# Optimization experiments

Measured on AMD Instinct MI355X. Metric: run time of the kernel, lower is better.

The kernel has to match this reference:

```python
import jax, jax.numpy as jnp
import numpy as np

B, C, D, H, W = 4, 128, 16, 16, 16
C8 = C // 8
TEXT = 256
N = D * H * W


def setup_inputs() -> dict:
    key = jax.random.key(0)
    ks = jax.random.split(key, 13)
    s = lambda fan: 1.0 / np.sqrt(fan)
    return {
        "x": jax.random.normal(ks[0], (B, C, D, H, W), jnp.float32),
        "text_emb": jax.random.normal(ks[1], (B, TEXT), jnp.float32),
        "Wq": jax.random.normal(ks[2], (C8, C), jnp.float32) * s(C),
        "bq": jax.random.normal(ks[3], (C8,), jnp.float32) * 0.01,
        "Wk": jax.random.normal(ks[4], (C8, C), jnp.float32) * s(C),
        "bk": jax.random.normal(ks[5], (C8,), jnp.float32) * 0.01,
        "Wv": jax.random.normal(ks[6], (C, C), jnp.float32) * s(C),
        "bv": jax.random.normal(ks[7], (C,), jnp.float32) * 0.01,
        "Wtk": jax.random.normal(ks[8], (C8, TEXT), jnp.float32) * s(TEXT),
        "btk": jax.random.normal(ks[9], (C8,), jnp.float32) * 0.01,
        "Wtv": jax.random.normal(ks[10], (C, TEXT), jnp.float32) * s(TEXT),
        "btv": jax.random.normal(ks[11], (C,), jnp.float32) * 0.01,
        # gamma is zero-init in the original; use a nonzero value so the
        # attention path contributes to the output (and to gradients).
        "gamma": jax.random.normal(ks[12], (1,), jnp.float32) * 0.1 + 0.5,
    }


def reference(x, text_emb, Wq, bq, Wk, bk, Wv, bv, Wtk, btk, Wtv, btv, gamma):
    b, c, d, h, w = x.shape
    n = d * h * w
    xf = x.reshape(b, c, n)                       # [B, C, N]
    # 1x1x1 convs == channel matmuls
    q = jnp.einsum('oc,bcn->bno', Wq, xf) + bq    # [B, N, C8]
    k = jnp.einsum('oc,bcn->bon', Wk, xf) + bk[None, :, None]  # [B, C8, N]
    v = jnp.einsum('oc,bcn->bon', Wv, xf) + bv[None, :, None]  # [B, C, N]
    # text-conditioned additive key/value (broadcast over all voxels)
    tk = (text_emb @ Wtk.T + btk)[:, :, None]     # [B, C8, 1]
    tv = (text_emb @ Wtv.T + btv)[:, :, None]     # [B, C, 1]
    k = k + tk
    v = v + tv
    # unscaled attention: softmax over keys
    scores = jnp.einsum('bno,bom->bnm', q, k)     # [B, N, N]
    attn = jax.nn.softmax(scores, axis=-1)
    # out[b,c,n] = sum_m v[b,c,m] * attn[b,n,m]
    out = jnp.einsum('bcm,bnm->bcn', v, attn).reshape(b, c, d, h, w)
    return gamma * out + x
```

## Files before the change

kernel.cpp:

```cpp
#include <hip/hip_runtime.h>
#include <math.h>

#define BB 4
#define CC 128
#define C8 16
#define TEXTN 256
#define NN 4096
#define WQB 64
#define NT 32

typedef __attribute__((ext_vector_type(8))) __bf16 bf16x8;
typedef __attribute__((ext_vector_type(16))) float f32x16;

#define LOG2E 1.44269504088896340736f

static __device__ __forceinline__ ushort f2bf(float f) {
  unsigned u = __builtin_bit_cast(unsigned, f);
  u += 0x7FFFu + ((u >> 16) & 1u);
  return (ushort)(u >> 16);
}

static __device__ __forceinline__ float exp2a(float x) {
#if __has_builtin(__builtin_amdgcn_exp2f)
  return __builtin_amdgcn_exp2f(x);
#else
  return exp2f(x);
#endif
}

static __device__ __forceinline__ unsigned cvt_pk_bf16(float lo, float hi) {
  unsigned r;
  asm("v_cvt_pk_bf16_f32 %0, %1, %2" : "=v"(r) : "v"(lo), "v"(hi));
  return r;
}
static __device__ __forceinline__ void pl32swap(unsigned &a, unsigned &b) {
  asm("v_permlane32_swap_b32 %0, %1" : "+v"(a), "+v"(b));
}

#define SB() __builtin_amdgcn_sched_barrier(0)

__global__ __launch_bounds__(256) void k_text(
    const float* __restrict__ text, const float* __restrict__ Wtk,
    const float* __restrict__ btk, const float* __restrict__ Wtv,
    const float* __restrict__ btv, float* __restrict__ tkv) {
  __shared__ float ts[TEXTN];
  int b = blockIdx.x;
  for (int i = threadIdx.x; i < TEXTN; i += 256) ts[i] = text[b * TEXTN + i];
  __syncthreads();
  int o = threadIdx.x;
  if (o < 144) {
    const float* w;
    float acc;
    if (o < 16) { w = Wtk + o * TEXTN; acc = btk[o]; }
    else        { w = Wtv + (o - 16) * TEXTN; acc = btv[o - 16]; }
    #pragma unroll 8
    for (int t = 0; t < TEXTN; t++) acc += w[t] * ts[t];
    tkv[b * 144 + o] = acc;
  }
}

__global__ __launch_bounds__(320) void k_qkv(
    const float* __restrict__ x,
    const float* __restrict__ Wq, const float* __restrict__ bq,
    const float* __restrict__ Wk, const float* __restrict__ bk,
    const float* __restrict__ Wv, const float* __restrict__ bv,
    const float* __restrict__ tkv,
    ushort* __restrict__ qt, ushort* __restrict__ kt, ushort* __restrict__ vtB) {
  __shared__ __align__(16) ushort xs[64 * 128];
  int b = blockIdx.x >> 6;
  int n0 = (blockIdx.x & 63) * 64;
  int t = threadIdx.x;
  int w = t >> 6, lane = t & 63, l31 = lane & 31, hi = lane >> 5;

  for (int i = t; i < 1024; i += 320) {
    int n = i & 63, ch = i >> 6;
    union { ushort u[8]; uint4 v; } pk;
    #pragma unroll
    for (int j = 0; j < 8; ++j)
      pk.u[j] = f2bf(x[((size_t)b * CC + ch * 8 + j) * NN + n0 + n]);
    *(uint4*)&xs[n * 128 + ((ch ^ (n & 15)) << 3)] = pk.v;
  }

  const float* wrow;
  if (w == 0) wrow = (l31 < 16) ? (Wq + l31 * CC) : (Wk + (l31 - 16) * CC);
  else        wrow = Wv + (size_t)(32 * (w - 1) + l31) * CC;
  bf16x8 af[8];
  #pragma unroll
  for (int ks = 0; ks < 8; ++ks) {
    float4 u0 = *(const float4*)&wrow[ks * 16 + hi * 8];
    float4 u1 = *(const float4*)&wrow[ks * 16 + hi * 8 + 4];
    union { ushort u[8]; bf16x8 v; } tmp;
    tmp.u[0] = f2bf(u0.x); tmp.u[1] = f2bf(u0.y); tmp.u[2] = f2bf(u0.z); tmp.u[3] = f2bf(u0.w);
    tmp.u[4] = f2bf(u1.x); tmp.u[5] = f2bf(u1.y); tmp.u[6] = f2bf(u1.z); tmp.u[7] = f2bf(u1.w);
    af[ks] = tmp.v;
  }
  float badd[16];
  #pragma unroll
  for (int r = 0; r < 16; ++r) {
    int ol = (r & 3) + 8 * (r >> 2) + 4 * hi;
    if (w == 0) badd[r] = (ol < 16) ? bq[ol] : (bk[ol - 16] + tkv[b * 144 + ol - 16]);
    else { int c = 32 * (w - 1) + ol; badd[r] = bv[c] + tkv[b * 144 + 16 + c]; }
  }
  __syncthreads();

  #pragma unroll
  for (int n32 = 0; n32 < 2; ++n32) {
    int n = n32 * 32 + l31;
    int ng = n0 + n;
    bf16x8 bf[8];
    #pragma unroll
    for (int ks = 0; ks < 8; ++ks)
      bf[ks] = *(const bf16x8*)&xs[n * 128 + (((ks * 2 + hi) ^ (n & 15)) << 3)];
    f32x16 d;
    #pragma unroll
    for (int r = 0; r < 16; ++r) d[r] = 0.f;
    #pragma unroll
    for (int ks = 0; ks < 8; ++ks)
      d = __builtin_amdgcn_mfma_f32_32x32x16_bf16(af[ks], bf[ks], d, 0, 0, 0);
    #pragma unroll
    for (int g = 0; g < 4; ++g) {
      int o0 = 8 * g + 4 * hi;
      float v0 = d[g * 4 + 0] + badd[g * 4 + 0];
      float v1 = d[g * 4 + 1] + badd[g * 4 + 1];
      float v2 = d[g * 4 + 2] + badd[g * 4 + 2];
      float v3 = d[g * 4 + 3] + badd[g * 4 + 3];
      if (w == 0 && o0 < 16) { v0 *= LOG2E; v1 *= LOG2E; v2 *= LOG2E; v3 *= LOG2E; }
      ushort4 pkv;
      pkv.x = f2bf(v0); pkv.y = f2bf(v1); pkv.z = f2bf(v2); pkv.w = f2bf(v3);
      if (w == 0) {
        if (o0 < 16) *(ushort4*)&qt[(b * NN + ng) * C8 + o0] = pkv;
        else         *(ushort4*)&kt[(b * NN + ng) * C8 + o0 - 16] = pkv;
      } else {
        int c0 = 32 * (w - 1) + o0;
        int base = b * (NN / 8) * CC * 8 + (ng >> 3) * (CC * 8) + (ng & 7);
        vtB[base + (c0 + 0) * 8] = pkv.x;
        vtB[base + (c0 + 1) * 8] = pkv.y;
        vtB[base + (c0 + 2) * 8] = pkv.z;
        vtB[base + (c0 + 3) * 8] = pkv.w;
      }
    }
  }
}

__global__ __launch_bounds__(512) void k_attn(
    const ushort* __restrict__ qt, const ushort* __restrict__ kt,
    const ushort* __restrict__ vtB, const float* __restrict__ x,
    const float* __restrict__ gamma_p, float* __restrict__ out) {
  __shared__ __align__(16) float mergeAcc[4][2][1024];
  __shared__ float mergeL[4][2][2][32];
  __shared__ float invGL[64];

  int raw = blockIdx.x;
  int xcd = raw & 7, slot = raw >> 3;
  int b = xcd >> 1;
  int q0 = ((xcd & 1) * 32 + slot) * WQB;

  int t = threadIdx.x;
  int w = t >> 6, lane = t & 63, l31 = lane & 31, hi = lane >> 5;
  int ms = w >> 1, ch = w & 1;

  const ushort* ktb = kt + (size_t)b * NN * C8;
  const ushort* vbb = vtB + (size_t)b * (NN / 8) * CC * 8;

  bf16x8 qfA = *(const bf16x8*)&qt[((size_t)b * NN + q0 + l31) * C8 + hi * 8];
  bf16x8 qfB = *(const bf16x8*)&qt[((size_t)b * NN + q0 + 32 + l31) * C8 + hi * 8];

  f32x16 accA0, accA1, accB0, accB1;
  #pragma unroll
  for (int r = 0; r < 16; ++r) { accA0[r] = 0.f; accA1[r] = 0.f; accB0[r] = 0.f; accB1[r] = 0.f; }
  float lpA = 0.f, lpB = 0.f;

  f32x16 z;
  #pragma unroll
  for (int r = 0; r < 16; ++r) z[r] = 0.f;

  const ushort* kp  = ktb + (ms * 32 + l31) * C8 + hi * 8;
  const ushort* vp0 = vbb + (size_t)(ms * 4 + 0 + hi) * (CC * 8) + (ch * 64 + l31) * 8;
  const ushort* vp1 = vbb + (size_t)(ms * 4 + 2 + hi) * (CC * 8) + (ch * 64 + l31) * 8;

  bf16x8 kfA, kfB;
  bf16x8 vE0, vE1, vE2, vE3;
  bf16x8 vO0, vO1, vO2, vO3;
  bf16x8 paE0, paE1, pbE0, pbE1;
  bf16x8 paO0, paO1, pbO0, pbO1;


#define EXPCHUNK(S, BASE, PF, LP)                                             \
  {                                                                           \
    float p0 = exp2a(S[BASE + 0]), p1 = exp2a(S[BASE + 1]);                   \
    float p2 = exp2a(S[BASE + 2]), p3 = exp2a(S[BASE + 3]);                   \
    float p4 = exp2a(S[BASE + 4]), p5 = exp2a(S[BASE + 5]);                   \
    float p6 = exp2a(S[BASE + 6]), p7 = exp2a(S[BASE + 7]);                   \
    LP += ((p0 + p1) + (p2 + p3)) + ((p4 + p5) + (p6 + p7));                  \
    unsigned a = cvt_pk_bf16(p0, p1), bq_ = cvt_pk_bf16(p4, p5);              \
    unsigned c = cvt_pk_bf16(p2, p3), d = cvt_pk_bf16(p6, p7);                \
    pl32swap(a, bq_); pl32swap(c, d);                                         \
    union { unsigned u[4]; bf16x8 v; } uu;                                    \
    uu.u[0] = a; uu.u[1] = c; uu.u[2] = bq_; uu.u[3] = d;                     \
    PF = uu.v;                                                                \
  }

#define PVPAIR(Va, Vb, U, Aa, Ab)                                             \
  {                                                                           \
    __builtin_amdgcn_s_setprio(1);                                            \
    Aa = __builtin_amdgcn_mfma_f32_32x32x16_bf16(Va, U, Aa, 0, 0, 0);         \
    Ab = __builtin_amdgcn_mfma_f32_32x32x16_bf16(Vb, U, Ab, 0, 0, 0);         \
    __builtin_amdgcn_s_setprio(0);                                            \
  }

#define LOADV(L0, L1, L2, L3)                                                 \
    L0 = *(const bf16x8*)(vp0); L1 = *(const bf16x8*)(vp0 + 256);             \
    L2 = *(const bf16x8*)(vp1); L3 = *(const bf16x8*)(vp1 + 256);             \
    vp0 += 16 * CC * 8; vp1 += 16 * CC * 8;

#define STEP(KC, KN, VL0,VL1,VL2,VL3, VU0,VU1,VU2,VU3,                        \
             UA0,UA1,UB0,UB1, PA0,PA1,PB0,PB1)                                \
  {                                                                           \
    LOADV(VL0, VL1, VL2, VL3)                                                 \
    KN = *(const bf16x8*)kp; kp += 128 * C8;                                  \
    SB();                                                                     \
    f32x16 sA = __builtin_amdgcn_mfma_f32_32x32x16_bf16(KC, qfA, z, 0, 0, 0); \
    f32x16 sB = __builtin_amdgcn_mfma_f32_32x32x16_bf16(KC, qfB, z, 0, 0, 0); \
    SB();                                                                     \
    PVPAIR(VU0, VU1, UA0, accA0, accA1)                                       \
    SB();                                                                     \
    EXPCHUNK(sA, 0, PA0, lpA)                                                 \
    SB();                                                                     \
    PVPAIR(VU0, VU1, UB0, accB0, accB1)                                       \
    SB();                                                                     \
    EXPCHUNK(sA, 8, PA1, lpA)                                                 \
    SB();                                                                     \
    PVPAIR(VU2, VU3, UA1, accA0, accA1)                                       \
    SB();                                                                     \
    EXPCHUNK(sB, 0, PB0, lpB)                                                 \
    SB();                                                                     \
    PVPAIR(VU2, VU3, UB1, accB0, accB1)                                       \
    SB();                                                                     \
    EXPCHUNK(sB, 8, PB1, lpB)                                                 \
    SB();                                                                     \
  }

  kfA = *(const bf16x8*)kp; kp += 128 * C8;
  LOADV(vE0, vE1, vE2, vE3)
  kfB = *(const bf16x8*)kp; kp += 128 * C8;
  {
    f32x16 sA = __builtin_amdgcn_mfma_f32_32x32x16_bf16(kfA, qfA, z, 0, 0, 0);
    f32x16 sB = __builtin_amdgcn_mfma_f32_32x32x16_bf16(kfA, qfB, z, 0, 0, 0);
    EXPCHUNK(sA, 0, paE0, lpA)
    EXPCHUNK(sA, 8, paE1, lpA)
    EXPCHUNK(sB, 0, pbE0, lpB)
    EXPCHUNK(sB, 8, pbE1, lpB)
  }

  for (int tt = 1; tt <= 29; tt += 2) {
    STEP(kfB, kfA, vO0,vO1,vO2,vO3, vE0,vE1,vE2,vE3,
         paE0,paE1,pbE0,pbE1, paO0,paO1,pbO0,pbO1)
    STEP(kfA, kfB, vE0,vE1,vE2,vE3, vO0,vO1,vO2,vO3,
         paO0,paO1,pbO0,pbO1, paE0,paE1,pbE0,pbE1)
  }

  STEP(kfB, kfA, vO0,vO1,vO2,vO3, vE0,vE1,vE2,vE3,
       paE0,paE1,pbE0,pbE1, paO0,paO1,pbO0,pbO1)

  PVPAIR(vO0, vO1, paO0, accA0, accA1)
  PVPAIR(vO0, vO1, pbO0, accB0, accB1)
  PVPAIR(vO2, vO3, paO1, accA0, accA1)
  PVPAIR(vO2, vO3, pbO1, accB0, accB1)

#undef STEP
#undef PVPAIR
#undef EXPCHUNK
#undef LOADV

  if (ch == 0) {
    mergeL[ms][hi][0][l31] = lpA;
    mergeL[ms][hi][1][l31] = lpB;
  }
  __syncthreads();
  if (t < 64) {
    float L = 0.f;
    #pragma unroll
    for (int m2 = 0; m2 < 4; ++m2)
      #pragma unroll
      for (int h2 = 0; h2 < 2; ++h2) L += mergeL[m2][h2][t >> 5][t & 31];
    invGL[t] = gamma_p[0] / L;
  }

#define EPI(ACC, QT, CB, FIRST)                                               \
  {                                                                           \
    if (!(FIRST)) __syncthreads();                                            \
    _Pragma("unroll")                                                         \
    for (int r = 0; r < 16; ++r)                                              \
      mergeAcc[ms][ch][(((r & 3) + 8 * (r >> 2) + 4 * hi) << 5) | l31] = ACC[r]; \
    __syncthreads();                                                          \
    int idx = t * 4;                                                          \
    int qq = idx & 31, cl = idx >> 5;                                         \
    int chh = cl >> 5, crow = cl & 31;                                        \
    float4 sum = *(const float4*)&mergeAcc[0][chh][crow * 32 + qq];           \
    _Pragma("unroll")                                                         \
    for (int m2 = 1; m2 < 4; ++m2) {                                          \
      float4 sv = *(const float4*)&mergeAcc[m2][chh][crow * 32 + qq];         \
      sum.x += sv.x; sum.y += sv.y; sum.z += sv.z; sum.w += sv.w;             \
    }                                                                         \
    float4 gl = *(const float4*)&invGL[(QT) * 32 + qq];                       \
    int c = chh * 64 + (CB) * 32 + crow;                                      \
    size_t base = ((size_t)b * CC + c) * NN + q0 + (QT) * 32 + qq;            \
    float4 xv = *(const float4*)&x[base];                                     \
    float4 ov;                                                                \
    ov.x = sum.x * gl.x + xv.x;                                               \
    ov.y = sum.y * gl.y + xv.y;                                               \
    ov.z = sum.z * gl.z + xv.z;                                               \
    ov.w = sum.w * gl.w + xv.w;                                               \
    *(float4*)&out[base] = ov;                                                \
  }

  EPI(accA0, 0, 0, 1)
  EPI(accA1, 0, 1, 0)
  EPI(accB0, 1, 0, 0)
  EPI(accB1, 1, 1, 0)
#undef EPI
}

extern "C" void kernel_launch(void* const* d_in, const int* in_sizes, int n_in,
                              void* d_out, int out_size, void* d_ws, size_t ws_size,
                              hipStream_t stream) {
  const float* x     = (const float*)d_in[0];
  const float* text  = (const float*)d_in[1];
  const float* Wq    = (const float*)d_in[2];
  const float* bq    = (const float*)d_in[3];
  const float* Wk    = (const float*)d_in[4];
  const float* bk    = (const float*)d_in[5];
  const float* Wv    = (const float*)d_in[6];
  const float* bv    = (const float*)d_in[7];
  const float* Wtk   = (const float*)d_in[8];
  const float* btk   = (const float*)d_in[9];
  const float* Wtv   = (const float*)d_in[10];
  const float* btv   = (const float*)d_in[11];
  const float* gamma = (const float*)d_in[12];
  float* outp = (float*)d_out;

  char* wsb = (char*)d_ws;
  float*  tkv = (float*)wsb;
  ushort* qt  = (ushort*)(wsb + 4096);
  ushort* kt  = (ushort*)(wsb + 4096 + 524288);
  ushort* vtB = (ushort*)(wsb + 4096 + 2 * 524288);

  k_text<<<BB, 256, 0, stream>>>(text, Wtk, btk, Wtv, btv, tkv);
  k_qkv<<<BB * NN / 64, 320, 0, stream>>>(x, Wq, bq, Wk, bk, Wv, bv, tkv, qt, kt, vtB);
  k_attn<<<BB * (NN / WQB), 512, 0, stream>>>(qt, kt, vtB, x, gamma, outp);
}
```

Baseline: 50.54 us.

## Fuse text projection into QKV kernel and halve voxel tile per block

Removes the separate k_text launch: every k_qkv block now loads the text embedding into shared memory and computes the 144 text key/value offsets itself before adding them to the biases. The voxel tile per block drops from 64 to 32, doubling the grid to 512 blocks so more CUs are busy. This saves a kernel launch and a serialized dependency, at the cost of redundantly recomputing the 144x256 text matvec in every block and an extra barrier.

```diff
diff --git a/kernel.cpp b/kernel.cpp
--- a/kernel.cpp
+++ b/kernel.cpp
@@ -39,41 +39,26 @@
 
 #define SB() __builtin_amdgcn_sched_barrier(0)
 
-__global__ __launch_bounds__(256) void k_text(
-    const float* __restrict__ text, const float* __restrict__ Wtk,
-    const float* __restrict__ btk, const float* __restrict__ Wtv,
-    const float* __restrict__ btv, float* __restrict__ tkv) {
-  __shared__ float ts[TEXTN];
-  int b = blockIdx.x;
-  for (int i = threadIdx.x; i < TEXTN; i += 256) ts[i] = text[b * TEXTN + i];
-  __syncthreads();
-  int o = threadIdx.x;
-  if (o < 144) {
-    const float* w;
-    float acc;
-    if (o < 16) { w = Wtk + o * TEXTN; acc = btk[o]; }
-    else        { w = Wtv + (o - 16) * TEXTN; acc = btv[o - 16]; }
-    #pragma unroll 8
-    for (int t = 0; t < TEXTN; t++) acc += w[t] * ts[t];
-    tkv[b * 144 + o] = acc;
-  }
-}
-
 __global__ __launch_bounds__(320) void k_qkv(
-    const float* __restrict__ x,
+    const float* __restrict__ x, const float* __restrict__ text,
     const float* __restrict__ Wq, const float* __restrict__ bq,
     const float* __restrict__ Wk, const float* __restrict__ bk,
     const float* __restrict__ Wv, const float* __restrict__ bv,
-    const float* __restrict__ tkv,
+    const float* __restrict__ Wtk, const float* __restrict__ btk,
+    const float* __restrict__ Wtv, const float* __restrict__ btv,
     ushort* __restrict__ qt, ushort* __restrict__ kt, ushort* __restrict__ vtB) {
-  __shared__ __align__(16) ushort xs[64 * 128];
-  int b = blockIdx.x >> 6;
-  int n0 = (blockIdx.x & 63) * 64;
+  __shared__ __align__(16) ushort xs[32 * 128];
+  __shared__ __align__(16) float ts[TEXTN];
+  __shared__ float tkvS[144];
+
+  int b = blockIdx.x >> 7;
+  int n0 = (blockIdx.x & 127) * 32;
   int t = threadIdx.x;
   int w = t >> 6, lane = t & 63, l31 = lane & 31, hi = lane >> 5;
 
-  for (int i = t; i < 1024; i += 320) {
-    int n = i & 63, ch = i >> 6;
+  if (t < TEXTN) ts[t] = text[b * TEXTN + t];
+  for (int i = t; i < 512; i += 320) {
+    int n = i & 31, ch = i >> 5;
     union { ushort u[8]; uint4 v; } pk;
     #pragma unroll
     for (int j = 0; j < 8; ++j)
@@ -94,18 +79,32 @@
     tmp.u[4] = f2bf(u1.x); tmp.u[5] = f2bf(u1.y); tmp.u[6] = f2bf(u1.z); tmp.u[7] = f2bf(u1.w);
     af[ks] = tmp.v;
   }
+  __syncthreads();
+
+  if (t < 144) {
+    const float* wr = (t < 16) ? (Wtk + (size_t)t * TEXTN)
+                               : (Wtv + (size_t)(t - 16) * TEXTN);
+    float acc = (t < 16) ? btk[t] : btv[t - 16];
+    #pragma unroll 8
+    for (int j = 0; j < TEXTN / 4; ++j) {
+      float4 wv = *(const float4*)&wr[j * 4];
+      float4 tv = *(const float4*)&ts[j * 4];
+      acc += wv.x * tv.x + wv.y * tv.y + wv.z * tv.z + wv.w * tv.w;
+    }
+    tkvS[t] = acc;
+  }
+  __syncthreads();
+
   float badd[16];
   #pragma unroll
   for (int r = 0; r < 16; ++r) {
     int ol = (r & 3) + 8 * (r >> 2) + 4 * hi;
-    if (w == 0) badd[r] = (ol < 16) ? bq[ol] : (bk[ol - 16] + tkv[b * 144 + ol - 16]);
-    else { int c = 32 * (w - 1) + ol; badd[r] = bv[c] + tkv[b * 144 + 16 + c]; }
-  }
-  __syncthreads();
-
-  #pragma unroll
-  for (int n32 = 0; n32 < 2; ++n32) {
-    int n = n32 * 32 + l31;
+    if (w == 0) badd[r] = (ol < 16) ? bq[ol] : (bk[ol - 16] + tkvS[ol - 16]);
+    else { int c = 32 * (w - 1) + ol; badd[r] = bv[c] + tkvS[16 + c]; }
+  }
+
+  {
+    int n = l31;
     int ng = n0 + n;
     bf16x8 bf[8];
     #pragma unroll
@@ -340,12 +339,11 @@
   float* outp = (float*)d_out;
 
   char* wsb = (char*)d_ws;
-  float*  tkv = (float*)wsb;
   ushort* qt  = (ushort*)(wsb + 4096);
   ushort* kt  = (ushort*)(wsb + 4096 + 524288);
   ushort* vtB = (ushort*)(wsb + 4096 + 2 * 524288);
 
-  k_text<<<BB, 256, 0, stream>>>(text, Wtk, btk, Wtv, btv, tkv);
-  k_qkv<<<BB * NN / 64, 320, 0, stream>>>(x, Wq, bq, Wk, bk, Wv, bv, tkv, qt, kt, vtB);
+  k_qkv<<<BB * NN / 32, 320, 0, stream>>>(x, text, Wq, bq, Wk, bk, Wv, bv,
+                                          Wtk, btk, Wtv, btv, qt, kt, vtB);
   k_attn<<<BB * (NN / WQB), 512, 0, stream>>>(qt, kt, vtB, x, gamma, outp);
 }
```

New measurement: 51.72 us. 1.02x slower.
